# Performance work log

Hardware: AMD Instinct MI355X
Metric: run time of the kernel (lower is better)

Reference implementation:

```python
import jax, jax.numpy as jnp
import numpy as np

TOP_K = 8
ROUTED_SCALING = 2.5


def setup_inputs() -> dict:
    key = jax.random.key(0)
    ks = jax.random.split(key, 8)
    B, S, H, E, I = 2, 1024, 2048, 32, 1024
    IS = 2 * I  # shared expert intermediate (n_shared_experts * moe_intermediate_size)
    w = lambda k, shape: jax.random.normal(k, shape, dtype=jnp.float32) * 0.02
    return {
        "hidden_states": jax.random.normal(ks[0], (B, S, H), dtype=jnp.float32),
        "gate_weight": w(ks[1], (E, H)),
        "w_gate": w(ks[2], (E, H, I)),
        "w_up": w(ks[3], (E, H, I)),
        "w_down": w(ks[4], (E, I, H)),
        "ws_gate": w(ks[5], (H, IS)),
        "ws_up": w(ks[6], (H, IS)),
        "ws_down": w(ks[7], (IS, H)),
    }


def reference(hidden_states, gate_weight, w_gate, w_up, w_down, ws_gate, ws_up, ws_down):
    B, S, H = hidden_states.shape
    x = hidden_states.reshape(-1, H)  # [T, H]
    T = x.shape[0]
    E = gate_weight.shape[0]

    # --- gate (DeepseekV3 top-k router: sigmoid scores, top-k, renormalize, scale) ---
    scores = jax.nn.sigmoid(x @ gate_weight.T)              # [T, E]
    topk_w, topk_i = jax.lax.top_k(scores, TOP_K)           # [T, K]
    topk_w = topk_w / (jnp.sum(topk_w, axis=-1, keepdims=True) + 1e-20)
    topk_w = topk_w * ROUTED_SCALING

    # dense [T, E] combine weights (scatter of top-k weights; zeros elsewhere)
    dense_w = jnp.zeros((T, E), dtype=topk_w.dtype).at[
        jnp.arange(T)[:, None], topk_i
    ].add(topk_w)

    # --- all experts on all tokens (calibrate_all_experts semantics; non-selected get weight 0) ---
    g = jnp.einsum('th,ehi->eti', x, w_gate)                # [E, T, I]
    u = jnp.einsum('th,ehi->eti', x, w_up)                  # [E, T, I]
    eo = jnp.einsum('eti,eih->eth', jax.nn.silu(g) * u, w_down)  # [E, T, H]
    routed = jnp.einsum('eth,te->th', eo, dense_w)          # weighted scatter-combine

    # --- shared expert (gated SiLU MLP on residual) ---
    shared = (jax.nn.silu(x @ ws_gate) * (x @ ws_up)) @ ws_down

    return (routed + shared).reshape(B, S, H)
```

## Files before the change

kernel.cpp:

```cpp
#include <hip/hip_runtime.h>

#define T_TOK 2048
#define H_DIM 2048
#define E_NUM 32
#define I_DIM 1024
#define IS_DIM 2048
#define K_TOT (E_NUM * I_DIM + IS_DIM)
#define SLOT_CAP 2048
#define NE_ALL 34
#define GU_TILES 192
#define DN_TILES 176
#define ACT_SLOTS 24576

typedef __bf16 bf16x8 __attribute__((ext_vector_type(8)));
typedef float  f32x4  __attribute__((ext_vector_type(4)));
static_assert(sizeof(bf16x8) == 16, "bf16x8 must be 16B");

#define OFF_CNT   ((size_t)0)
#define OFF_NTGU  ((size_t)192)
#define OFF_NTDN  ((size_t)196)
#define OFF_BASE  ((size_t)256)
#define OFF_TGU   ((size_t)512)
#define OFF_TDN   ((size_t)1280)
#define OFF_PAIRS ((size_t)2048)
#define OFF_XB    ((size_t)280576)
#define OFF_WGT   ((size_t)8669184)
#define OFF_PO    OFF_WGT
#define OFF_WUT   ((size_t)142886912)
#define OFF_WSGT  ((size_t)277104640)
#define OFF_WSUT  ((size_t)285493248)
#define OFF_WDT   ((size_t)293881856)
#define OFF_ACT   ((size_t)436488192)
#define OFF_TSLOT ((size_t)486819840)

__device__ __forceinline__ unsigned short f2bf(float f) {
  unsigned int u = __float_as_uint(f);
  u += 0x7fffu + ((u >> 16) & 1u);
  return (unsigned short)(u >> 16);
}

__device__ __forceinline__ void gld16(const void* g, void* l) {
  __builtin_amdgcn_global_load_lds(
      (const __attribute__((address_space(1))) unsigned int*)g,
      (__attribute__((address_space(3))) unsigned int*)l, 16, 0, 0);
}

__global__ __launch_bounds__(256) void router_kernel(
    const float* __restrict__ x, const float* __restrict__ gw,
    int* __restrict__ cnt, unsigned int* __restrict__ pairs,
    unsigned int* __restrict__ tslot, unsigned short* __restrict__ xb)
{
  const int t = blockIdx.x;
  __shared__ float xs[H_DIM];
  __shared__ float sc[E_NUM];
  const float4* xr = (const float4*)(x + (long)t * H_DIM);
  for (int i = threadIdx.x; i < H_DIM / 4; i += 256) ((float4*)xs)[i] = xr[i];
  __syncthreads();
  {
    const int i0 = threadIdx.x * 8;
    ushort4 o1, o2;
    o1.x = f2bf(xs[i0 + 0]); o1.y = f2bf(xs[i0 + 1]);
    o1.z = f2bf(xs[i0 + 2]); o1.w = f2bf(xs[i0 + 3]);
    o2.x = f2bf(xs[i0 + 4]); o2.y = f2bf(xs[i0 + 5]);
    o2.z = f2bf(xs[i0 + 6]); o2.w = f2bf(xs[i0 + 7]);
    *(ushort4*)(xb + (long)t * H_DIM + i0) = o1;
    *(ushort4*)(xb + (long)t * H_DIM + i0 + 4) = o2;
  }
  const int e = threadIdx.x >> 3, p = threadIdx.x & 7;
  const float4* ga = (const float4*)(gw + (long)e * H_DIM);
  const float4* xa = (const float4*)xs;
  float s = 0.f;
  #pragma unroll 4
  for (int i = p * 64; i < p * 64 + 64; ++i) {
    float4 a = ga[i], b = xa[i];
    s += a.x * b.x + a.y * b.y + a.z * b.z + a.w * b.w;
  }
  s += __shfl_down(s, 4, 8);
  s += __shfl_down(s, 2, 8);
  s += __shfl_down(s, 1, 8);
  if (p == 0) sc[e] = 1.f / (1.f + expf(-s));
  __syncthreads();
  if (threadIdx.x == 0) {
    float v[E_NUM];
    #pragma unroll
    for (int i = 0; i < E_NUM; ++i) v[i] = sc[i];
    unsigned mask = 0; float sum = 0.f;
    int sel[8]; float wv[8];
    for (int k = 0; k < 8; ++k) {
      float best = -1.f; int bi = 0;
      for (int i = 0; i < E_NUM; ++i)
        if (!((mask >> i) & 1u) && v[i] > best) { best = v[i]; bi = i; }
      mask |= 1u << bi; sel[k] = bi; wv[k] = best; sum += best;
    }
    const float scale = 2.5f / (sum + 1e-20f);
    for (int k = 0; k < 8; ++k) {
      const int slot = atomicAdd(&cnt[sel[k]], 1);
      if (slot < SLOT_CAP) {
        const unsigned int w16 = (unsigned int)f2bf(wv[k] * scale);
        pairs[sel[k] * SLOT_CAP + slot] = (w16 << 16) | (unsigned int)t;
        tslot[t * 8 + k] = ((unsigned int)sel[k] << 16) | (unsigned int)slot;
      }
    }
  }
}

__global__ __launch_bounds__(256) void build_tiles_kernel(
    int* __restrict__ cnt, int* __restrict__ base,
    unsigned int* __restrict__ tgu, int* __restrict__ ntgu,
    unsigned int* __restrict__ tdn, int* __restrict__ ntdn,
    unsigned int* __restrict__ pairs)
{
  const int t = threadIdx.x;
  for (int s = t; s < T_TOK; s += 256) {
    const unsigned int pv = (0x3F80u << 16) | (unsigned int)s;
    pairs[32 * SLOT_CAP + s] = pv;
    pairs[33 * SLOT_CAP + s] = pv;
  }
  if (t == 0) {
    cnt[32] = T_TOK; cnt[33] = T_TOK;
    int b = 0, ngu = 0, ndn = 0;
    for (int e = 0; e < NE_ALL; ++e) {
      const int c = (e < 32) ? cnt[e] : T_TOK;
      base[e] = b;
      for (int m0 = 0; m0 < c; m0 += 128) {
        tgu[ngu++] = ((unsigned int)e << 16) | (unsigned int)m0;
        if (e < 33) tdn[ndn++] = ((unsigned int)e << 16) | (unsigned int)m0;
      }
      b += (c + 127) & ~127;
    }
    *ntgu = ngu; *ntdn = ndn;
  }
}

struct TDescTable {
  const float* in[6];
  unsigned short* out[6];
  int C[6];
  int ldout[6];
  long in_bs[6];
  long out_bs[6];
  int nbx[6];
  int nbxy[6];
  int start[7];
};

__global__ __launch_bounds__(256) void transpose_fused(TDescTable td)
{
  const int bid = blockIdx.x;
  int i = 0;
  while (i < 5 && bid >= td.start[i + 1]) ++i;
  const int local = bid - td.start[i];
  const int bz = local / td.nbxy[i];
  const int rem = local % td.nbxy[i];
  const int by = rem / td.nbx[i];
  const int bx = rem % td.nbx[i];
  const float* in = td.in[i] + (long)bz * td.in_bs[i];
  unsigned short* out = td.out[i] + (long)bz * td.out_bs[i];
  const int C = td.C[i], ldout = td.ldout[i];

  __shared__ unsigned short tile[64][258];
  const int c0 = bx * 64;
  const int r0 = by * 256;
  const int t = threadIdx.x;
  const int rl0 = t >> 4;
  const int cl0 = (t & 15) * 4;

  float4 v[16];
  #pragma unroll
  for (int p = 0; p < 16; ++p) {
    const int rl = p * 16 + rl0;
    v[p] = *(const float4*)(in + (long)(r0 + rl) * C + c0 + cl0);
  }
  __builtin_amdgcn_sched_barrier(0);
  #pragma unroll
  for (int p = 0; p < 16; ++p) {
    const int rl = p * 16 + rl0;
    tile[cl0 + 0][rl] = f2bf(v[p].x);
    tile[cl0 + 1][rl] = f2bf(v[p].y);
    tile[cl0 + 2][rl] = f2bf(v[p].z);
    tile[cl0 + 3][rl] = f2bf(v[p].w);
  }
  __syncthreads();
  const int cw = t >> 5;
  const int rw = (t & 31) * 8;
  #pragma unroll
  for (int q = 0; q < 8; ++q) {
    const int cl = q * 8 + cw;
    const char* src = (const char*)&tile[cl][rw];
    uint4 o;
    o.x = *(const unsigned int*)(src + 0);
    o.y = *(const unsigned int*)(src + 4);
    o.z = *(const unsigned int*)(src + 8);
    o.w = *(const unsigned int*)(src + 12);
    *(uint4*)(out + (long)(c0 + cl) * ldout + r0 + rw) = o;
  }
}

__global__ __launch_bounds__(256) void gate_up_moe_kernel(
    const unsigned short* __restrict__ xb,
    const unsigned short* __restrict__ bgT,
    const unsigned short* __restrict__ buT,
    const unsigned short* __restrict__ sgT,
    const unsigned short* __restrict__ suT,
    const int* __restrict__ cnt,
    const int* __restrict__ base,
    const unsigned int* __restrict__ pairs,
    const unsigned int* __restrict__ tiles,
    const int* __restrict__ ntp,
    unsigned short* __restrict__ act)
{
  const int ti = blockIdx.y;
  if (ti >= *ntp) return;
  const unsigned int tile = tiles[ti];
  const int e  = (int)(tile >> 16);
  const int m0 = (int)(tile & 0xFFFFu);
  const int cnte = cnt[e];
  const int be = base[e];
  const int n0 = blockIdx.x * 64;
  const long panel = (long)I_DIM * H_DIM;
  const unsigned short* Bg =
      ((e < 32) ? bgT + e * panel : sgT + (e - 32) * panel) + (long)n0 * H_DIM;
  const unsigned short* Bu =
      ((e < 32) ? buT + e * panel : suT + (e - 32) * panel) + (long)n0 * H_DIM;

  __shared__ unsigned short sA[128 * 64];
  __shared__ unsigned short sBg[64 * 64];
  __shared__ unsigned short sBu[64 * 64];

  const int tid = threadIdx.x;
  const int lane = tid & 63;
  const int wid = tid >> 6;
  const int wm = wid >> 1, wn = wid & 1;
  const int l15 = lane & 15;
  const int lk  = (lane >> 4) * 8;
  const int srow = tid >> 3;
  const int scol = (tid & 7) * 8;
  const int scolsw = (((tid & 7) ^ (srow & 7))) * 8;
  const int ksw = (l15 & 7) << 3;

  const unsigned short* asrc[4];
  #pragma unroll
  for (int r = 0; r < 4; ++r) {
    const int slot = m0 + r * 32 + srow;
    const unsigned int pr = (slot < cnte) ? pairs[e * SLOT_CAP + slot] : 0u;
    asrc[r] = xb + (long)(pr & 0xFFFFu) * H_DIM + scolsw;
  }

  const f32x4 fz = {0.f, 0.f, 0.f, 0.f};
  f32x4 accg[4][2], accu[4][2];
  #pragma unroll
  for (int i = 0; i < 4; ++i)
    #pragma unroll
    for (int j = 0; j < 2; ++j) { accg[i][j] = fz; accu[i][j] = fz; }

  for (int k0 = 0; k0 < H_DIM; k0 += 64) {
    #pragma unroll
    for (int r = 0; r < 4; ++r)
      gld16(asrc[r] + k0, sA + (r * 32 + srow) * 64 + scol);
    #pragma unroll
    for (int r = 0; r < 2; ++r) {
      gld16(Bg + (long)(r * 32 + srow) * H_DIM + k0 + scolsw,
            sBg + (r * 32 + srow) * 64 + scol);
      gld16(Bu + (long)(r * 32 + srow) * H_DIM + k0 + scolsw,
            sBu + (r * 32 + srow) * 64 + scol);
    }
    __syncthreads();
    __builtin_amdgcn_s_setprio(1);
    #pragma unroll
    for (int kk = 0; kk < 2; ++kk) {
      const int ko = kk * 32 + lk;
      bf16x8 a[4], g[2], u[2];
      #pragma unroll
      for (int mi = 0; mi < 4; ++mi)
        a[mi] = *(const bf16x8*)(sA + (wm * 64 + mi * 16 + l15) * 64 + (ko ^ ksw));
      #pragma unroll
      for (int ni = 0; ni < 2; ++ni) {
        g[ni] = *(const bf16x8*)(sBg + (wn * 32 + ni * 16 + l15) * 64 + (ko ^ ksw));
        u[ni] = *(const bf16x8*)(sBu + (wn * 32 + ni * 16 + l15) * 64 + (ko ^ ksw));
      }
      #pragma unroll
      for (int mi = 0; mi < 4; ++mi)
        #pragma unroll
        for (int ni = 0; ni < 2; ++ni) {
          accg[mi][ni] = __builtin_amdgcn_mfma_f32_16x16x32_bf16(a[mi], g[ni], accg[mi][ni], 0, 0, 0);
          accu[mi][ni] = __builtin_amdgcn_mfma_f32_16x16x32_bf16(a[mi], u[ni], accu[mi][ni], 0, 0, 0);
        }
    }
    __builtin_amdgcn_s_setprio(0);
    __syncthreads();
  }

  const int colb = n0 + wn * 32;
  #pragma unroll
  for (int mi = 0; mi < 4; ++mi) {
    #pragma unroll
    for (int r = 0; r < 4; ++r) {
      const int slot = m0 + wm * 64 + mi * 16 + (lane >> 4) * 4 + r;
      if (slot < cnte) {
        const unsigned int pr = pairs[e * SLOT_CAP + slot];
        const float w = __uint_as_float(pr & 0xFFFF0000u);
        #pragma unroll
        for (int ni = 0; ni < 2; ++ni) {
          const float gv = accg[mi][ni][r];
          const float uv = accu[mi][ni][r];
          const float sv = (gv / (1.f + expf(-gv))) * uv * w;
          act[((long)(be + slot)) * I_DIM + colb + ni * 16 + l15] = f2bf(sv);
        }
      }
    }
  }
}

__global__ __launch_bounds__(256) void down_moe_kernel(
    const unsigned short* __restrict__ act,
    const unsigned short* __restrict__ wdT,
    const int* __restrict__ cnt,
    const int* __restrict__ base,
    const unsigned int* __restrict__ tiles,
    const int* __restrict__ ntp,
    unsigned short* __restrict__ po)
{
  const int ti = blockIdx.y;
  if (ti >= *ntp) return;
  const unsigned int tile = tiles[ti];
  const int e  = (int)(tile >> 16);
  const int m0 = (int)(tile & 0xFFFFu);
  const int cnte = cnt[e];
  const int be = base[e];
  const int n0 = blockIdx.x * 128;
  const unsigned short* A = act + ((long)be + m0) * I_DIM;
  const unsigned short* B = wdT + (long)n0 * K_TOT + (long)e * I_DIM;
  const int nk = (e == 32) ? 32 : 16;

  __shared__ unsigned short sA[128 * 64];
  __shared__ unsigned short sB[128 * 64];

  const int tid = threadIdx.x;
  const int lane = tid & 63;
  const int wid = tid >> 6;
  const int wm = wid >> 1, wn = wid & 1;
  const int l15 = lane & 15;
  const int lk  = (lane >> 4) * 8;
  const int srow = tid >> 3;
  const int scol = (tid & 7) * 8;
  const int scolsw = (((tid & 7) ^ (srow & 7))) * 8;
  const int ksw = (l15 & 7) << 3;

  const f32x4 fz = {0.f, 0.f, 0.f, 0.f};
  f32x4 acc[4][4];
  #pragma unroll
  for (int i = 0; i < 4; ++i)
    #pragma unroll
    for (int j = 0; j < 4; ++j) acc[i][j] = fz;

  for (int t = 0; t < nk; ++t) {
    const int k0 = t * 64;
    const long koff = (long)(k0 & 1023) + (long)(k0 >> 10) * (2048L * 1024L);
    #pragma unroll
    for (int r = 0; r < 4; ++r)
      gld16(A + (long)(r * 32 + srow) * I_DIM + koff + scolsw,
            sA + (r * 32 + srow) * 64 + scol);
    #pragma unroll
    for (int r = 0; r < 4; ++r)
      gld16(B + (long)(r * 32 + srow) * K_TOT + k0 + scolsw,
            sB + (r * 32 + srow) * 64 + scol);
    __syncthreads();
    __builtin_amdgcn_s_setprio(1);
    #pragma unroll
    for (int kk = 0; kk < 2; ++kk) {
      const int ko = kk * 32 + lk;
      bf16x8 a[4], b[4];
      #pragma unroll
      for (int mi = 0; mi < 4; ++mi)
        a[mi] = *(const bf16x8*)(sA + (wm * 64 + mi * 16 + l15) * 64 + (ko ^ ksw));
      #pragma unroll
      for (int ni = 0; ni < 4; ++ni)
        b[ni] = *(const bf16x8*)(sB + (wn * 64 + ni * 16 + l15) * 64 + (ko ^ ksw));
      #pragma unroll
      for (int mi = 0; mi < 4; ++mi)
        #pragma unroll
        for (int ni = 0; ni < 4; ++ni)
          acc[mi][ni] = __builtin_amdgcn_mfma_f32_16x16x32_bf16(a[mi], b[ni], acc[mi][ni], 0, 0, 0);
    }
    __builtin_amdgcn_s_setprio(0);
    __syncthreads();
  }

  #pragma unroll
  for (int mi = 0; mi < 4; ++mi) {
    #pragma unroll
    for (int r = 0; r < 4; ++r) {
      const int slot = m0 + wm * 64 + mi * 16 + (lane >> 4) * 4 + r;
      if (slot < cnte) {
        unsigned short* pr = po + (long)(be + slot) * H_DIM + n0 + wn * 64;
        #pragma unroll
        for (int ni = 0; ni < 4; ++ni)
          pr[ni * 16 + l15] = f2bf(acc[mi][ni][r]);
      }
    }
  }
}

__global__ __launch_bounds__(256) void combine_kernel(
    const unsigned short* __restrict__ po,
    const int* __restrict__ base,
    const unsigned int* __restrict__ tslot,
    float* __restrict__ out)
{
  const int t = blockIdx.x;
  __shared__ int rows[9];
  if (threadIdx.x < 8) {
    const unsigned int pr = tslot[t * 8 + threadIdx.x];
    rows[threadIdx.x] = base[pr >> 16] + (int)(pr & 0xFFFFu);
  }
  if (threadIdx.x == 8) rows[8] = base[32] + t;
  __syncthreads();
  const int col = threadIdx.x * 8;
  float s[8];
  #pragma unroll
  for (int j = 0; j < 8; ++j) s[j] = 0.f;
  #pragma unroll
  for (int k = 0; k < 9; ++k) {
    const ushort4* p = (const ushort4*)(po + (long)rows[k] * H_DIM + col);
    const ushort4 v0 = p[0], v1 = p[1];
    s[0] += __uint_as_float((unsigned int)v0.x << 16);
    s[1] += __uint_as_float((unsigned int)v0.y << 16);
    s[2] += __uint_as_float((unsigned int)v0.z << 16);
    s[3] += __uint_as_float((unsigned int)v0.w << 16);
    s[4] += __uint_as_float((unsigned int)v1.x << 16);
    s[5] += __uint_as_float((unsigned int)v1.y << 16);
    s[6] += __uint_as_float((unsigned int)v1.z << 16);
    s[7] += __uint_as_float((unsigned int)v1.w << 16);
  }
  float4 o0 = {s[0], s[1], s[2], s[3]};
  float4 o1 = {s[4], s[5], s[6], s[7]};
  *(float4*)(out + (long)t * H_DIM + col) = o0;
  *(float4*)(out + (long)t * H_DIM + col + 4) = o1;
}

extern "C" void kernel_launch(void* const* d_in, const int* in_sizes, int n_in,
                              void* d_out, int out_size, void* d_ws, size_t ws_size,
                              hipStream_t stream) {
  (void)in_sizes; (void)n_in; (void)out_size; (void)ws_size;
  const float* x   = (const float*)d_in[0];
  const float* gw  = (const float*)d_in[1];
  const float* wg  = (const float*)d_in[2];
  const float* wu  = (const float*)d_in[3];
  const float* wd  = (const float*)d_in[4];
  const float* wsg = (const float*)d_in[5];
  const float* wsu = (const float*)d_in[6];
  const float* wsd = (const float*)d_in[7];
  float* out = (float*)d_out;
  char* ws = (char*)d_ws;

  int*            cnt   = (int*)(ws + OFF_CNT);
  int*            ntgu  = (int*)(ws + OFF_NTGU);
  int*            ntdn  = (int*)(ws + OFF_NTDN);
  int*            basep = (int*)(ws + OFF_BASE);
  unsigned int*   tgu   = (unsigned int*)(ws + OFF_TGU);
  unsigned int*   tdn   = (unsigned int*)(ws + OFF_TDN);
  unsigned int*   pairs = (unsigned int*)(ws + OFF_PAIRS);
  unsigned int*   tslot = (unsigned int*)(ws + OFF_TSLOT);
  unsigned short* xb    = (unsigned short*)(ws + OFF_XB);
  unsigned short* wgT   = (unsigned short*)(ws + OFF_WGT);
  unsigned short* wuT   = (unsigned short*)(ws + OFF_WUT);
  unsigned short* wsgT  = (unsigned short*)(ws + OFF_WSGT);
  unsigned short* wsuT  = (unsigned short*)(ws + OFF_WSUT);
  unsigned short* wdT   = (unsigned short*)(ws + OFF_WDT);
  unsigned short* actb  = (unsigned short*)(ws + OFF_ACT);
  unsigned short* pob   = (unsigned short*)(ws + OFF_PO);

  hipMemsetAsync(ws + OFF_CNT, 0, 256, stream);

  router_kernel<<<T_TOK, 256, 0, stream>>>(x, gw, cnt, pairs, tslot, xb);
  build_tiles_kernel<<<1, 256, 0, stream>>>(cnt, basep, tgu, ntgu, tdn, ntdn,
                                            pairs);

  TDescTable ta;
  ta.in[0] = wg;  ta.out[0] = wgT;  ta.C[0] = I_DIM;  ta.ldout[0] = H_DIM;
  ta.in_bs[0] = (long)H_DIM * I_DIM; ta.out_bs[0] = (long)I_DIM * H_DIM;
  ta.nbx[0] = I_DIM / 64; ta.nbxy[0] = (I_DIM / 64) * (H_DIM / 256);
  ta.in[1] = wu;  ta.out[1] = wuT;  ta.C[1] = I_DIM;  ta.ldout[1] = H_DIM;
  ta.in_bs[1] = (long)H_DIM * I_DIM; ta.out_bs[1] = (long)I_DIM * H_DIM;
  ta.nbx[1] = I_DIM / 64; ta.nbxy[1] = (I_DIM / 64) * (H_DIM / 256);
  ta.in[2] = wsg; ta.out[2] = wsgT; ta.C[2] = IS_DIM; ta.ldout[2] = H_DIM;
  ta.in_bs[2] = 0; ta.out_bs[2] = 0;
  ta.nbx[2] = IS_DIM / 64; ta.nbxy[2] = (IS_DIM / 64) * (H_DIM / 256);
  ta.in[3] = wsu; ta.out[3] = wsuT; ta.C[3] = IS_DIM; ta.ldout[3] = H_DIM;
  ta.in_bs[3] = 0; ta.out_bs[3] = 0;
  ta.nbx[3] = IS_DIM / 64; ta.nbxy[3] = (IS_DIM / 64) * (H_DIM / 256);
  for (int i = 4; i < 6; ++i) {
    ta.in[i] = ta.in[3]; ta.out[i] = ta.out[3]; ta.C[i] = ta.C[3];
    ta.ldout[i] = ta.ldout[3]; ta.in_bs[i] = 0; ta.out_bs[i] = 0;
    ta.nbx[i] = 1; ta.nbxy[i] = 1;
  }
  ta.start[0] = 0;
  ta.start[1] = ta.start[0] + ta.nbxy[0] * E_NUM;
  ta.start[2] = ta.start[1] + ta.nbxy[1] * E_NUM;
  ta.start[3] = ta.start[2] + ta.nbxy[2];
  ta.start[4] = ta.start[3] + ta.nbxy[3];
  ta.start[5] = ta.start[4];
  ta.start[6] = ta.start[4];
  transpose_fused<<<ta.start[4], 256, 0, stream>>>(ta);

  gate_up_moe_kernel<<<dim3(16, GU_TILES), 256, 0, stream>>>(
      xb, wgT, wuT, wsgT, wsuT, cnt, basep, pairs, tgu, ntgu, actb);

  TDescTable tb;
  tb.in[0] = wd;  tb.out[0] = wdT;  tb.C[0] = H_DIM;  tb.ldout[0] = K_TOT;
  tb.in_bs[0] = (long)I_DIM * H_DIM; tb.out_bs[0] = (long)I_DIM;
  tb.nbx[0] = H_DIM / 64; tb.nbxy[0] = (H_DIM / 64) * (I_DIM / 256);
  tb.in[1] = wsd; tb.out[1] = wdT + E_NUM * I_DIM; tb.C[1] = H_DIM;
  tb.ldout[1] = K_TOT; tb.in_bs[1] = 0; tb.out_bs[1] = 0;
  tb.nbx[1] = H_DIM / 64; tb.nbxy[1] = (H_DIM / 64) * (IS_DIM / 256);
  for (int i = 2; i < 6; ++i) {
    tb.in[i] = tb.in[1]; tb.out[i] = tb.out[1]; tb.C[i] = tb.C[1];
    tb.ldout[i] = tb.ldout[1]; tb.in_bs[i] = 0; tb.out_bs[i] = 0;
    tb.nbx[i] = 1; tb.nbxy[i] = 1;
  }
  tb.start[0] = 0;
  tb.start[1] = tb.start[0] + tb.nbxy[0] * E_NUM;
  tb.start[2] = tb.start[1] + tb.nbxy[1];
  tb.start[3] = tb.start[2];
  tb.start[4] = tb.start[2];
  tb.start[5] = tb.start[2];
  tb.start[6] = tb.start[2];
  transpose_fused<<<tb.start[2], 256, 0, stream>>>(tb);

  down_moe_kernel<<<dim3(16, DN_TILES), 256, 0, stream>>>(
      actb, wdT, cnt, basep, tdn, ntdn, pob);

  combine_kernel<<<T_TOK, 256, 0, stream>>>(pob, basep, tslot, out);
}
```

Measured before the change: 753.4 us.

## Pipeline MoE GEMMs with triple-buffered LDS and 256-row tiles over 512 threads

Both grouped MoE GEMM kernels (gate/up and down) now use 256-token M tiles and 512-thread blocks. Their K loops use a three-stage LDS ring filled by async global-to-LDS loads, with explicit vmcnt waits and split barriers so loads for step t+2 overlap MFMA work on step t. This aims to hide global load latency and reuse weights across more tokens per block. In exchange LDS use grows a lot, which may lower occupancy, and expert segments are padded to 256 rows, which adds wasted work on partly filled tiles.

```diff
diff --git a/kernel.cpp b/kernel.cpp
--- a/kernel.cpp
+++ b/kernel.cpp
@@ -8,9 +8,9 @@
 #define K_TOT (E_NUM * I_DIM + IS_DIM)
 #define SLOT_CAP 2048
 #define NE_ALL 34
-#define GU_TILES 192
-#define DN_TILES 176
-#define ACT_SLOTS 24576
+#define GU2_TILES 128
+#define DN2_TILES 112
+#define ACT_SLOTS 28672
 
 typedef __bf16 bf16x8 __attribute__((ext_vector_type(8)));
 typedef float  f32x4  __attribute__((ext_vector_type(4)));
@@ -31,7 +31,7 @@
 #define OFF_WSUT  ((size_t)285493248)
 #define OFF_WDT   ((size_t)293881856)
 #define OFF_ACT   ((size_t)436488192)
-#define OFF_TSLOT ((size_t)486819840)
+#define OFF_TSLOT ((size_t)495208448)
 
 __device__ __forceinline__ unsigned short f2bf(float f) {
   unsigned int u = __float_as_uint(f);
@@ -44,6 +44,8 @@
       (const __attribute__((address_space(1))) unsigned int*)g,
       (__attribute__((address_space(3))) unsigned int*)l, 16, 0, 0);
 }
+
+#define WAITV(N) asm volatile("s_waitcnt vmcnt(" #N ")" ::: "memory")
 
 __global__ __launch_bounds__(256) void router_kernel(
     const float* __restrict__ x, const float* __restrict__ gw,
@@ -122,11 +124,11 @@
     for (int e = 0; e < NE_ALL; ++e) {
       const int c = (e < 32) ? cnt[e] : T_TOK;
       base[e] = b;
-      for (int m0 = 0; m0 < c; m0 += 128) {
+      for (int m0 = 0; m0 < c; m0 += 256) {
         tgu[ngu++] = ((unsigned int)e << 16) | (unsigned int)m0;
         if (e < 33) tdn[ndn++] = ((unsigned int)e << 16) | (unsigned int)m0;
       }
-      b += (c + 127) & ~127;
+      b += (c + 255) & ~255;
     }
     *ntgu = ngu; *ntdn = ndn;
   }
@@ -196,7 +198,7 @@
   }
 }
 
-__global__ __launch_bounds__(256) void gate_up_moe_kernel(
+__global__ __launch_bounds__(512) void gate_up_moe_kernel(
     const unsigned short* __restrict__ xb,
     const unsigned short* __restrict__ bgT,
     const unsigned short* __restrict__ buT,
@@ -223,9 +225,9 @@
   const unsigned short* Bu =
       ((e < 32) ? buT + e * panel : suT + (e - 32) * panel) + (long)n0 * H_DIM;
 
-  __shared__ unsigned short sA[128 * 64];
-  __shared__ unsigned short sBg[64 * 64];
-  __shared__ unsigned short sBu[64 * 64];
+  __shared__ unsigned short sA[3 * 256 * 64];
+  __shared__ unsigned short sBg[3 * 64 * 64];
+  __shared__ unsigned short sBu[3 * 64 * 64];
 
   const int tid = threadIdx.x;
   const int lane = tid & 63;
@@ -241,7 +243,7 @@
   const unsigned short* asrc[4];
   #pragma unroll
   for (int r = 0; r < 4; ++r) {
-    const int slot = m0 + r * 32 + srow;
+    const int slot = m0 + r * 64 + srow;
     const unsigned int pr = (slot < cnte) ? pairs[e * SLOT_CAP + slot] : 0u;
     asrc[r] = xb + (long)(pr & 0xFFFFu) * H_DIM + scolsw;
   }
@@ -253,42 +255,65 @@
     #pragma unroll
     for (int j = 0; j < 2; ++j) { accg[i][j] = fz; accu[i][j] = fz; }
 
-  for (int k0 = 0; k0 < H_DIM; k0 += 64) {
-    #pragma unroll
-    for (int r = 0; r < 4; ++r)
-      gld16(asrc[r] + k0, sA + (r * 32 + srow) * 64 + scol);
-    #pragma unroll
-    for (int r = 0; r < 2; ++r) {
-      gld16(Bg + (long)(r * 32 + srow) * H_DIM + k0 + scolsw,
-            sBg + (r * 32 + srow) * 64 + scol);
-      gld16(Bu + (long)(r * 32 + srow) * H_DIM + k0 + scolsw,
-            sBu + (r * 32 + srow) * 64 + scol);
-    }
-    __syncthreads();
-    __builtin_amdgcn_s_setprio(1);
-    #pragma unroll
-    for (int kk = 0; kk < 2; ++kk) {
-      const int ko = kk * 32 + lk;
-      bf16x8 a[4], g[2], u[2];
-      #pragma unroll
-      for (int mi = 0; mi < 4; ++mi)
-        a[mi] = *(const bf16x8*)(sA + (wm * 64 + mi * 16 + l15) * 64 + (ko ^ ksw));
-      #pragma unroll
-      for (int ni = 0; ni < 2; ++ni) {
-        g[ni] = *(const bf16x8*)(sBg + (wn * 32 + ni * 16 + l15) * 64 + (ko ^ ksw));
-        u[ni] = *(const bf16x8*)(sBu + (wn * 32 + ni * 16 + l15) * 64 + (ko ^ ksw));
-      }
-      #pragma unroll
-      for (int mi = 0; mi < 4; ++mi)
-        #pragma unroll
-        for (int ni = 0; ni < 2; ++ni) {
-          accg[mi][ni] = __builtin_amdgcn_mfma_f32_16x16x32_bf16(a[mi], g[ni], accg[mi][ni], 0, 0, 0);
-          accu[mi][ni] = __builtin_amdgcn_mfma_f32_16x16x32_bf16(a[mi], u[ni], accu[mi][ni], 0, 0, 0);
-        }
-    }
-    __builtin_amdgcn_s_setprio(0);
-    __syncthreads();
-  }
+#define STG_A(buf, k0, r)                                                      \
+    gld16(asrc[r] + (k0), sA + (buf) * 16384 + ((r) * 64 + srow) * 64 + scol)
+#define STG_BG(buf, k0)                                                        \
+    gld16(Bg + (long)srow * H_DIM + (k0) + scolsw,                             \
+          sBg + (buf) * 4096 + srow * 64 + scol)
+#define STG_BU(buf, k0)                                                        \
+    gld16(Bu + (long)srow * H_DIM + (k0) + scolsw,                             \
+          sBu + (buf) * 4096 + srow * 64 + scol)
+
+#define CLUSTER_GU(cb, kk) do {                                                \
+    const int ko = (kk) * 32 + lk;                                             \
+    bf16x8 a[4], g[2], u[2];                                                   \
+    _Pragma("unroll")                                                          \
+    for (int mi = 0; mi < 4; ++mi)                                             \
+      a[mi] = *(const bf16x8*)(sA + (cb) * 16384 +                             \
+               (wm * 64 + mi * 16 + l15) * 64 + (ko ^ ksw));                   \
+    _Pragma("unroll")                                                          \
+    for (int ni = 0; ni < 2; ++ni) {                                           \
+      g[ni] = *(const bf16x8*)(sBg + (cb) * 4096 +                             \
+               (wn * 32 + ni * 16 + l15) * 64 + (ko ^ ksw));                   \
+      u[ni] = *(const bf16x8*)(sBu + (cb) * 4096 +                             \
+               (wn * 32 + ni * 16 + l15) * 64 + (ko ^ ksw));                   \
+    }                                                                          \
+    __builtin_amdgcn_s_setprio(1);                                             \
+    _Pragma("unroll")                                                          \
+    for (int mi = 0; mi < 4; ++mi)                                             \
+      _Pragma("unroll")                                                        \
+      for (int ni = 0; ni < 2; ++ni) {                                         \
+        accg[mi][ni] = __builtin_amdgcn_mfma_f32_16x16x32_bf16(                \
+            a[mi], g[ni], accg[mi][ni], 0, 0, 0);                              \
+        accu[mi][ni] = __builtin_amdgcn_mfma_f32_16x16x32_bf16(                \
+            a[mi], u[ni], accu[mi][ni], 0, 0, 0);                              \
+      }                                                                        \
+    __builtin_amdgcn_s_setprio(0);                                             \
+  } while (0)
+
+  WAITV(0);
+  #pragma unroll
+  for (int p = 0; p < 2; ++p) {
+    const int k0 = p * 64;
+    STG_A(p, k0, 0); STG_A(p, k0, 1); STG_BG(p, k0);
+    STG_A(p, k0, 2); STG_A(p, k0, 3); STG_BU(p, k0);
+  }
+  for (int t = 0; t < 32; ++t) {
+    const int cb = t % 3;
+    const int pb = (t + 2) % 3;
+    const int k2 = (t + 2) * 64;
+    if (t + 1 < 32) { WAITV(6); } else { WAITV(0); }
+    __builtin_amdgcn_s_barrier();
+    if (t + 2 < 32) { STG_A(pb, k2, 0); STG_A(pb, k2, 1); STG_BG(pb, k2); }
+    CLUSTER_GU(cb, 0);
+    __builtin_amdgcn_s_barrier();
+    if (t + 2 < 32) { STG_A(pb, k2, 2); STG_A(pb, k2, 3); STG_BU(pb, k2); }
+    CLUSTER_GU(cb, 1);
+  }
+#undef STG_A
+#undef STG_BG
+#undef STG_BU
+#undef CLUSTER_GU
 
   const int colb = n0 + wn * 32;
   #pragma unroll
@@ -311,7 +336,7 @@
   }
 }
 
-__global__ __launch_bounds__(256) void down_moe_kernel(
+__global__ __launch_bounds__(512) void down_moe_kernel(
     const unsigned short* __restrict__ act,
     const unsigned short* __restrict__ wdT,
     const int* __restrict__ cnt,
@@ -332,8 +357,8 @@
   const unsigned short* B = wdT + (long)n0 * K_TOT + (long)e * I_DIM;
   const int nk = (e == 32) ? 32 : 16;
 
-  __shared__ unsigned short sA[128 * 64];
-  __shared__ unsigned short sB[128 * 64];
+  __shared__ unsigned short sA[3 * 256 * 64];
+  __shared__ unsigned short sB[3 * 128 * 64];
 
   const int tid = threadIdx.x;
   const int lane = tid & 63;
@@ -353,38 +378,58 @@
     #pragma unroll
     for (int j = 0; j < 4; ++j) acc[i][j] = fz;
 
+#define KOFF(k0) ((long)((k0) & 1023) + (long)((k0) >> 10) * (2048L * 1024L))
+#define STG_A(buf, k0, r)                                                      \
+    gld16(A + (long)((r) * 64 + srow) * I_DIM + KOFF(k0) + scolsw,             \
+          sA + (buf) * 16384 + ((r) * 64 + srow) * 64 + scol)
+#define STG_B(buf, k0, r)                                                      \
+    gld16(B + (long)((r) * 64 + srow) * K_TOT + (k0) + scolsw,                 \
+          sB + (buf) * 8192 + ((r) * 64 + srow) * 64 + scol)
+
+#define CLUSTER_DN(cb, kk) do {                                                \
+    const int ko = (kk) * 32 + lk;                                             \
+    bf16x8 a[4], b[4];                                                         \
+    _Pragma("unroll")                                                          \
+    for (int mi = 0; mi < 4; ++mi)                                             \
+      a[mi] = *(const bf16x8*)(sA + (cb) * 16384 +                             \
+               (wm * 64 + mi * 16 + l15) * 64 + (ko ^ ksw));                   \
+    _Pragma("unroll")                                                          \
+    for (int ni = 0; ni < 4; ++ni)                                             \
+      b[ni] = *(const bf16x8*)(sB + (cb) * 8192 +                              \
+               (wn * 64 + ni * 16 + l15) * 64 + (ko ^ ksw));                   \
+    __builtin_amdgcn_s_setprio(1);                                             \
+    _Pragma("unroll")                                                          \
+    for (int mi = 0; mi < 4; ++mi)                                             \
+      _Pragma("unroll")                                                        \
+      for (int ni = 0; ni < 4; ++ni)                                           \
+        acc[mi][ni] = __builtin_amdgcn_mfma_f32_16x16x32_bf16(                 \
+            a[mi], b[ni], acc[mi][ni], 0, 0, 0);                               \
+    __builtin_amdgcn_s_setprio(0);                                             \
+  } while (0)
+
+  WAITV(0);
+  #pragma unroll
+  for (int p = 0; p < 2; ++p) {
+    const int k0 = p * 64;
+    STG_A(p, k0, 0); STG_A(p, k0, 1); STG_B(p, k0, 0);
+    STG_A(p, k0, 2); STG_A(p, k0, 3); STG_B(p, k0, 1);
+  }
   for (int t = 0; t < nk; ++t) {
-    const int k0 = t * 64;
-    const long koff = (long)(k0 & 1023) + (long)(k0 >> 10) * (2048L * 1024L);
-    #pragma unroll
-    for (int r = 0; r < 4; ++r)
-      gld16(A + (long)(r * 32 + srow) * I_DIM + koff + scolsw,
-            sA + (r * 32 + srow) * 64 + scol);
-    #pragma unroll
-    for (int r = 0; r < 4; ++r)
-      gld16(B + (long)(r * 32 + srow) * K_TOT + k0 + scolsw,
-            sB + (r * 32 + srow) * 64 + scol);
-    __syncthreads();
-    __builtin_amdgcn_s_setprio(1);
-    #pragma unroll
-    for (int kk = 0; kk < 2; ++kk) {
-      const int ko = kk * 32 + lk;
-      bf16x8 a[4], b[4];
-      #pragma unroll
-      for (int mi = 0; mi < 4; ++mi)
-        a[mi] = *(const bf16x8*)(sA + (wm * 64 + mi * 16 + l15) * 64 + (ko ^ ksw));
-      #pragma unroll
-      for (int ni = 0; ni < 4; ++ni)
-        b[ni] = *(const bf16x8*)(sB + (wn * 64 + ni * 16 + l15) * 64 + (ko ^ ksw));
-      #pragma unroll
-      for (int mi = 0; mi < 4; ++mi)
-        #pragma unroll
-        for (int ni = 0; ni < 4; ++ni)
-          acc[mi][ni] = __builtin_amdgcn_mfma_f32_16x16x32_bf16(a[mi], b[ni], acc[mi][ni], 0, 0, 0);
-    }
-    __builtin_amdgcn_s_setprio(0);
-    __syncthreads();
-  }
+    const int cb = t % 3;
+    const int pb = (t + 2) % 3;
+    const int k2 = (t + 2) * 64;
+    if (t + 1 < nk) { WAITV(6); } else { WAITV(0); }
+    __builtin_amdgcn_s_barrier();
+    if (t + 2 < nk) { STG_A(pb, k2, 0); STG_A(pb, k2, 1); STG_B(pb, k2, 0); }
+    CLUSTER_DN(cb, 0);
+    __builtin_amdgcn_s_barrier();
+    if (t + 2 < nk) { STG_A(pb, k2, 2); STG_A(pb, k2, 3); STG_B(pb, k2, 1); }
+    CLUSTER_DN(cb, 1);
+  }
+#undef KOFF
+#undef STG_A
+#undef STG_B
+#undef CLUSTER_DN
 
   #pragma unroll
   for (int mi = 0; mi < 4; ++mi) {
@@ -503,7 +548,7 @@
   ta.start[6] = ta.start[4];
   transpose_fused<<<ta.start[4], 256, 0, stream>>>(ta);
 
-  gate_up_moe_kernel<<<dim3(16, GU_TILES), 256, 0, stream>>>(
+  gate_up_moe_kernel<<<dim3(16, GU2_TILES), 512, 0, stream>>>(
       xb, wgT, wuT, wsgT, wsuT, cnt, basep, pairs, tgu, ntgu, actb);
 
   TDescTable tb;
@@ -527,7 +572,7 @@
   tb.start[6] = tb.start[2];
   transpose_fused<<<tb.start[2], 256, 0, stream>>>(tb);
 
-  down_moe_kernel<<<dim3(16, DN_TILES), 256, 0, stream>>>(
+  down_moe_kernel<<<dim3(16, DN2_TILES), 512, 0, stream>>>(
       actb, wdT, cnt, basep, tdn, ntdn, pob);
 
   combine_kernel<<<T_TOK, 256, 0, stream>>>(pob, basep, tslot, out);
```

Result: slower. 1.062 ms (median of 2 runs) (+40.9%).

## Fuse down-proj weight transpose into gate/up GEMM kernel as interleaved blocks

Applied to the files above, without the earlier changes.

The separate transpose launch for w_down and ws_down is removed. That work now runs inside the gate/up MoE kernel: three of every four blockIdx.y rows do transpose tiles (128x64), and the fourth runs a GEMM tile. The aim is to overlap the memory-bound weight conversion with the compute-bound GEMM and drop one launch. The shared memory is unioned, and the grid grows 4x in y, with many early-exit blocks.

```diff
diff --git a/kernel.cpp b/kernel.cpp
--- a/kernel.cpp
+++ b/kernel.cpp
@@ -11,6 +11,8 @@
 #define GU_TILES 192
 #define DN_TILES 176
 #define ACT_SLOTS 24576
+#define TB_BLOCKS 8704
+#define TB_ROWS 544
 
 typedef __bf16 bf16x8 __attribute__((ext_vector_type(8)));
 typedef float  f32x4  __attribute__((ext_vector_type(4)));
@@ -133,22 +135,22 @@
 }
 
 struct TDescTable {
-  const float* in[6];
-  unsigned short* out[6];
-  int C[6];
-  int ldout[6];
-  long in_bs[6];
-  long out_bs[6];
-  int nbx[6];
-  int nbxy[6];
-  int start[7];
+  const float* in[4];
+  unsigned short* out[4];
+  int C[4];
+  int ldout[4];
+  long in_bs[4];
+  long out_bs[4];
+  int nbx[4];
+  int nbxy[4];
+  int start[5];
 };
 
-__global__ __launch_bounds__(256) void transpose_fused(TDescTable td)
+__global__ __launch_bounds__(256) void transpose_A(TDescTable td)
 {
   const int bid = blockIdx.x;
   int i = 0;
-  while (i < 5 && bid >= td.start[i + 1]) ++i;
+  while (i < 3 && bid >= td.start[i + 1]) ++i;
   const int local = bid - td.start[i];
   const int bz = local / td.nbxy[i];
   const int rem = local % td.nbxy[i];
@@ -196,7 +198,7 @@
   }
 }
 
-__global__ __launch_bounds__(256) void gate_up_moe_kernel(
+__global__ __launch_bounds__(256) void gate_up_tb_kernel(
     const unsigned short* __restrict__ xb,
     const unsigned short* __restrict__ bgT,
     const unsigned short* __restrict__ buT,
@@ -207,9 +209,70 @@
     const unsigned int* __restrict__ pairs,
     const unsigned int* __restrict__ tiles,
     const int* __restrict__ ntp,
-    unsigned short* __restrict__ act)
+    unsigned short* __restrict__ act,
+    const float* __restrict__ wd,
+    const float* __restrict__ wsd,
+    unsigned short* __restrict__ wdT)
 {
-  const int ti = blockIdx.y;
+  __shared__ unsigned short smem[16384];
+  const int y = blockIdx.y;
+
+  if ((y & 3) != 0) {
+    const int tpRow = y - (y >> 2) - 1;
+    if (tpRow >= TB_ROWS) return;
+    const int bid = tpRow * 16 + blockIdx.x;
+    const float* in;
+    unsigned short* out;
+    int by, bx;
+    if (bid < 8192) {
+      const int e = bid >> 8, rem = bid & 255;
+      by = rem >> 5; bx = rem & 31;
+      in = wd + (long)e * I_DIM * H_DIM;
+      out = wdT + (long)e * I_DIM;
+    } else {
+      const int b2 = bid - 8192;
+      by = b2 >> 5; bx = b2 & 31;
+      in = wsd;
+      out = wdT + E_NUM * I_DIM;
+    }
+    const int c0 = bx * 64, r0 = by * 128;
+    unsigned short (*tile)[130] = (unsigned short (*)[130])smem;
+    const int t = threadIdx.x;
+    const int rl0 = t >> 4;
+    const int cl0 = (t & 15) * 4;
+    float4 v[8];
+    #pragma unroll
+    for (int p = 0; p < 8; ++p) {
+      const int rl = p * 16 + rl0;
+      v[p] = *(const float4*)(in + (long)(r0 + rl) * H_DIM + c0 + cl0);
+    }
+    __builtin_amdgcn_sched_barrier(0);
+    #pragma unroll
+    for (int p = 0; p < 8; ++p) {
+      const int rl = p * 16 + rl0;
+      tile[cl0 + 0][rl] = f2bf(v[p].x);
+      tile[cl0 + 1][rl] = f2bf(v[p].y);
+      tile[cl0 + 2][rl] = f2bf(v[p].z);
+      tile[cl0 + 3][rl] = f2bf(v[p].w);
+    }
+    __syncthreads();
+    const int cw = t >> 4;
+    const int rw = (t & 15) * 8;
+    #pragma unroll
+    for (int q = 0; q < 4; ++q) {
+      const int cl = q * 16 + cw;
+      const char* src = (const char*)&tile[cl][rw];
+      uint4 o;
+      o.x = *(const unsigned int*)(src + 0);
+      o.y = *(const unsigned int*)(src + 4);
+      o.z = *(const unsigned int*)(src + 8);
+      o.w = *(const unsigned int*)(src + 12);
+      *(uint4*)(out + (long)(c0 + cl) * K_TOT + r0 + rw) = o;
+    }
+    return;
+  }
+
+  const int ti = y >> 2;
   if (ti >= *ntp) return;
   const unsigned int tile = tiles[ti];
   const int e  = (int)(tile >> 16);
@@ -223,9 +286,9 @@
   const unsigned short* Bu =
       ((e < 32) ? buT + e * panel : suT + (e - 32) * panel) + (long)n0 * H_DIM;
 
-  __shared__ unsigned short sA[128 * 64];
-  __shared__ unsigned short sBg[64 * 64];
-  __shared__ unsigned short sBu[64 * 64];
+  unsigned short* sA  = smem;
+  unsigned short* sBg = smem + 8192;
+  unsigned short* sBu = smem + 12288;
 
   const int tid = threadIdx.x;
   const int lane = tid & 63;
@@ -489,43 +552,16 @@
   ta.in[3] = wsu; ta.out[3] = wsuT; ta.C[3] = IS_DIM; ta.ldout[3] = H_DIM;
   ta.in_bs[3] = 0; ta.out_bs[3] = 0;
   ta.nbx[3] = IS_DIM / 64; ta.nbxy[3] = (IS_DIM / 64) * (H_DIM / 256);
-  for (int i = 4; i < 6; ++i) {
-    ta.in[i] = ta.in[3]; ta.out[i] = ta.out[3]; ta.C[i] = ta.C[3];
-    ta.ldout[i] = ta.ldout[3]; ta.in_bs[i] = 0; ta.out_bs[i] = 0;
-    ta.nbx[i] = 1; ta.nbxy[i] = 1;
-  }
   ta.start[0] = 0;
   ta.start[1] = ta.start[0] + ta.nbxy[0] * E_NUM;
   ta.start[2] = ta.start[1] + ta.nbxy[1] * E_NUM;
   ta.start[3] = ta.start[2] + ta.nbxy[2];
   ta.start[4] = ta.start[3] + ta.nbxy[3];
-  ta.start[5] = ta.start[4];
-  ta.start[6] = ta.start[4];
-  transpose_fused<<<ta.start[4], 256, 0, stream>>>(ta);
-
-  gate_up_moe_kernel<<<dim3(16, GU_TILES), 256, 0, stream>>>(
-      xb, wgT, wuT, wsgT, wsuT, cnt, basep, pairs, tgu, ntgu, actb);
-
-  TDescTable tb;
-  tb.in[0] = wd;  tb.out[0] = wdT;  tb.C[0] = H_DIM;  tb.ldout[0] = K_TOT;
-  tb.in_bs[0] = (long)I_DIM * H_DIM; tb.out_bs[0] = (long)I_DIM;
-  tb.nbx[0] = H_DIM / 64; tb.nbxy[0] = (H_DIM / 64) * (I_DIM / 256);
-  tb.in[1] = wsd; tb.out[1] = wdT + E_NUM * I_DIM; tb.C[1] = H_DIM;
-  tb.ldout[1] = K_TOT; tb.in_bs[1] = 0; tb.out_bs[1] = 0;
-  tb.nbx[1] = H_DIM / 64; tb.nbxy[1] = (H_DIM / 64) * (IS_DIM / 256);
-  for (int i = 2; i < 6; ++i) {
-    tb.in[i] = tb.in[1]; tb.out[i] = tb.out[1]; tb.C[i] = tb.C[1];
-    tb.ldout[i] = tb.ldout[1]; tb.in_bs[i] = 0; tb.out_bs[i] = 0;
-    tb.nbx[i] = 1; tb.nbxy[i] = 1;
-  }
-  tb.start[0] = 0;
-  tb.start[1] = tb.start[0] + tb.nbxy[0] * E_NUM;
-  tb.start[2] = tb.start[1] + tb.nbxy[1];
-  tb.start[3] = tb.start[2];
-  tb.start[4] = tb.start[2];
-  tb.start[5] = tb.start[2];
-  tb.start[6] = tb.start[2];
-  transpose_fused<<<tb.start[2], 256, 0, stream>>>(tb);
+  transpose_A<<<ta.start[4], 256, 0, stream>>>(ta);
+
+  gate_up_tb_kernel<<<dim3(16, 4 * GU_TILES), 256, 0, stream>>>(
+      xb, wgT, wuT, wsgT, wsuT, cnt, basep, pairs, tgu, ntgu, actb,
+      wd, wsd, wdT);
 
   down_moe_kernel<<<dim3(16, DN_TILES), 256, 0, stream>>>(
       actb, wdT, cnt, basep, tdn, ntdn, pob);
```

Result: slower. 867.6 us (+15.2%).

## Widen gate/up MoE tile to 128 columns with 512 threads; fuse transposes

Applied to the files above, without the earlier changes.

The gate/up grouped GEMM now computes a 128x128 output tile per block using 8 waves, so each loaded A (token) tile is reused across twice as many columns and the grid halves in x. The down-projection weight transpose is folded into the same transpose launch as the gate and up weights, removing one kernel launch. The larger tile raises LDS and register use per block, which can reduce occupancy.

```diff
diff --git a/kernel.cpp b/kernel.cpp
--- a/kernel.cpp
+++ b/kernel.cpp
@@ -196,7 +196,7 @@
   }
 }
 
-__global__ __launch_bounds__(256) void gate_up_moe_kernel(
+__global__ __launch_bounds__(512) void gate_up_moe_kernel(
     const unsigned short* __restrict__ xb,
     const unsigned short* __restrict__ bgT,
     const unsigned short* __restrict__ buT,
@@ -216,7 +216,7 @@
   const int m0 = (int)(tile & 0xFFFFu);
   const int cnte = cnt[e];
   const int be = base[e];
-  const int n0 = blockIdx.x * 64;
+  const int n0 = blockIdx.x * 128;
   const long panel = (long)I_DIM * H_DIM;
   const unsigned short* Bg =
       ((e < 32) ? bgT + e * panel : sgT + (e - 32) * panel) + (long)n0 * H_DIM;
@@ -224,13 +224,13 @@
       ((e < 32) ? buT + e * panel : suT + (e - 32) * panel) + (long)n0 * H_DIM;
 
   __shared__ unsigned short sA[128 * 64];
-  __shared__ unsigned short sBg[64 * 64];
-  __shared__ unsigned short sBu[64 * 64];
+  __shared__ unsigned short sBg[128 * 64];
+  __shared__ unsigned short sBu[128 * 64];
 
   const int tid = threadIdx.x;
   const int lane = tid & 63;
   const int wid = tid >> 6;
-  const int wm = wid >> 1, wn = wid & 1;
+  const int wm = wid >> 2, wn = wid & 3;
   const int l15 = lane & 15;
   const int lk  = (lane >> 4) * 8;
   const int srow = tid >> 3;
@@ -238,10 +238,10 @@
   const int scolsw = (((tid & 7) ^ (srow & 7))) * 8;
   const int ksw = (l15 & 7) << 3;
 
-  const unsigned short* asrc[4];
-  #pragma unroll
-  for (int r = 0; r < 4; ++r) {
-    const int slot = m0 + r * 32 + srow;
+  const unsigned short* asrc[2];
+  #pragma unroll
+  for (int r = 0; r < 2; ++r) {
+    const int slot = m0 + r * 64 + srow;
     const unsigned int pr = (slot < cnte) ? pairs[e * SLOT_CAP + slot] : 0u;
     asrc[r] = xb + (long)(pr & 0xFFFFu) * H_DIM + scolsw;
   }
@@ -255,14 +255,12 @@
 
   for (int k0 = 0; k0 < H_DIM; k0 += 64) {
     #pragma unroll
-    for (int r = 0; r < 4; ++r)
-      gld16(asrc[r] + k0, sA + (r * 32 + srow) * 64 + scol);
-    #pragma unroll
     for (int r = 0; r < 2; ++r) {
-      gld16(Bg + (long)(r * 32 + srow) * H_DIM + k0 + scolsw,
-            sBg + (r * 32 + srow) * 64 + scol);
-      gld16(Bu + (long)(r * 32 + srow) * H_DIM + k0 + scolsw,
-            sBu + (r * 32 + srow) * 64 + scol);
+      gld16(asrc[r] + k0, sA + (r * 64 + srow) * 64 + scol);
+      gld16(Bg + (long)(r * 64 + srow) * H_DIM + k0 + scolsw,
+            sBg + (r * 64 + srow) * 64 + scol);
+      gld16(Bu + (long)(r * 64 + srow) * H_DIM + k0 + scolsw,
+            sBu + (r * 64 + srow) * 64 + scol);
     }
     __syncthreads();
     __builtin_amdgcn_s_setprio(1);
@@ -476,56 +474,35 @@
   build_tiles_kernel<<<1, 256, 0, stream>>>(cnt, basep, tgu, ntgu, tdn, ntdn,
                                             pairs);
 
-  TDescTable ta;
-  ta.in[0] = wg;  ta.out[0] = wgT;  ta.C[0] = I_DIM;  ta.ldout[0] = H_DIM;
-  ta.in_bs[0] = (long)H_DIM * I_DIM; ta.out_bs[0] = (long)I_DIM * H_DIM;
-  ta.nbx[0] = I_DIM / 64; ta.nbxy[0] = (I_DIM / 64) * (H_DIM / 256);
-  ta.in[1] = wu;  ta.out[1] = wuT;  ta.C[1] = I_DIM;  ta.ldout[1] = H_DIM;
-  ta.in_bs[1] = (long)H_DIM * I_DIM; ta.out_bs[1] = (long)I_DIM * H_DIM;
-  ta.nbx[1] = I_DIM / 64; ta.nbxy[1] = (I_DIM / 64) * (H_DIM / 256);
-  ta.in[2] = wsg; ta.out[2] = wsgT; ta.C[2] = IS_DIM; ta.ldout[2] = H_DIM;
-  ta.in_bs[2] = 0; ta.out_bs[2] = 0;
-  ta.nbx[2] = IS_DIM / 64; ta.nbxy[2] = (IS_DIM / 64) * (H_DIM / 256);
-  ta.in[3] = wsu; ta.out[3] = wsuT; ta.C[3] = IS_DIM; ta.ldout[3] = H_DIM;
-  ta.in_bs[3] = 0; ta.out_bs[3] = 0;
-  ta.nbx[3] = IS_DIM / 64; ta.nbxy[3] = (IS_DIM / 64) * (H_DIM / 256);
-  for (int i = 4; i < 6; ++i) {
-    ta.in[i] = ta.in[3]; ta.out[i] = ta.out[3]; ta.C[i] = ta.C[3];
-    ta.ldout[i] = ta.ldout[3]; ta.in_bs[i] = 0; ta.out_bs[i] = 0;
-    ta.nbx[i] = 1; ta.nbxy[i] = 1;
-  }
-  ta.start[0] = 0;
-  ta.start[1] = ta.start[0] + ta.nbxy[0] * E_NUM;
-  ta.start[2] = ta.start[1] + ta.nbxy[1] * E_NUM;
-  ta.start[3] = ta.start[2] + ta.nbxy[2];
-  ta.start[4] = ta.start[3] + ta.nbxy[3];
-  ta.start[5] = ta.start[4];
-  ta.start[6] = ta.start[4];
-  transpose_fused<<<ta.start[4], 256, 0, stream>>>(ta);
-
-  gate_up_moe_kernel<<<dim3(16, GU_TILES), 256, 0, stream>>>(
+  TDescTable td;
+  td.in[0] = wg;  td.out[0] = wgT;  td.C[0] = I_DIM;  td.ldout[0] = H_DIM;
+  td.in_bs[0] = (long)H_DIM * I_DIM; td.out_bs[0] = (long)I_DIM * H_DIM;
+  td.nbx[0] = I_DIM / 64; td.nbxy[0] = (I_DIM / 64) * (H_DIM / 256);
+  td.in[1] = wu;  td.out[1] = wuT;  td.C[1] = I_DIM;  td.ldout[1] = H_DIM;
+  td.in_bs[1] = (long)H_DIM * I_DIM; td.out_bs[1] = (long)I_DIM * H_DIM;
+  td.nbx[1] = I_DIM / 64; td.nbxy[1] = (I_DIM / 64) * (H_DIM / 256);
+  td.in[2] = wd;  td.out[2] = wdT;  td.C[2] = H_DIM;  td.ldout[2] = K_TOT;
+  td.in_bs[2] = (long)I_DIM * H_DIM; td.out_bs[2] = (long)I_DIM;
+  td.nbx[2] = H_DIM / 64; td.nbxy[2] = (H_DIM / 64) * (I_DIM / 256);
+  td.in[3] = wsg; td.out[3] = wsgT; td.C[3] = IS_DIM; td.ldout[3] = H_DIM;
+  td.in_bs[3] = 0; td.out_bs[3] = 0;
+  td.nbx[3] = IS_DIM / 64; td.nbxy[3] = (IS_DIM / 64) * (H_DIM / 256);
+  td.in[4] = wsu; td.out[4] = wsuT; td.C[4] = IS_DIM; td.ldout[4] = H_DIM;
+  td.in_bs[4] = 0; td.out_bs[4] = 0;
+  td.nbx[4] = IS_DIM / 64; td.nbxy[4] = (IS_DIM / 64) * (H_DIM / 256);
+  td.in[5] = wsd; td.out[5] = wdT + E_NUM * I_DIM; td.C[5] = H_DIM;
+  td.ldout[5] = K_TOT; td.in_bs[5] = 0; td.out_bs[5] = 0;
+  td.nbx[5] = H_DIM / 64; td.nbxy[5] = (H_DIM / 64) * (IS_DIM / 256);
+  td.start[0] = 0;
+  for (int i = 0; i < 5; ++i) {
+    int nz = (i <= 2) ? E_NUM : 1;
+    td.start[i + 1] = td.start[i] + td.nbxy[i] * nz;
+  }
+  td.start[6] = td.start[5] + td.nbxy[5];
+  transpose_fused<<<td.start[6], 256, 0, stream>>>(td);
+
+  gate_up_moe_kernel<<<dim3(8, GU_TILES), 512, 0, stream>>>(
       xb, wgT, wuT, wsgT, wsuT, cnt, basep, pairs, tgu, ntgu, actb);
-
-  TDescTable tb;
-  tb.in[0] = wd;  tb.out[0] = wdT;  tb.C[0] = H_DIM;  tb.ldout[0] = K_TOT;
-  tb.in_bs[0] = (long)I_DIM * H_DIM; tb.out_bs[0] = (long)I_DIM;
-  tb.nbx[0] = H_DIM / 64; tb.nbxy[0] = (H_DIM / 64) * (I_DIM / 256);
-  tb.in[1] = wsd; tb.out[1] = wdT + E_NUM * I_DIM; tb.C[1] = H_DIM;
-  tb.ldout[1] = K_TOT; tb.in_bs[1] = 0; tb.out_bs[1] = 0;
-  tb.nbx[1] = H_DIM / 64; tb.nbxy[1] = (H_DIM / 64) * (IS_DIM / 256);
-  for (int i = 2; i < 6; ++i) {
-    tb.in[i] = tb.in[1]; tb.out[i] = tb.out[1]; tb.C[i] = tb.C[1];
-    tb.ldout[i] = tb.ldout[1]; tb.in_bs[i] = 0; tb.out_bs[i] = 0;
-    tb.nbx[i] = 1; tb.nbxy[i] = 1;
-  }
-  tb.start[0] = 0;
-  tb.start[1] = tb.start[0] + tb.nbxy[0] * E_NUM;
-  tb.start[2] = tb.start[1] + tb.nbxy[1];
-  tb.start[3] = tb.start[2];
-  tb.start[4] = tb.start[2];
-  tb.start[5] = tb.start[2];
-  tb.start[6] = tb.start[2];
-  transpose_fused<<<tb.start[2], 256, 0, stream>>>(tb);
 
   down_moe_kernel<<<dim3(16, DN_TILES), 256, 0, stream>>>(
       actb, wdT, cnt, basep, tdn, ntdn, pob);
```

Result: no change. 747.9 us (-0.7%).
